# Performance work log

Hardware: AMD Instinct MI355X
Metric: run time of the kernel (lower is better)

Reference implementation:

```python
import jax, jax.numpy as jnp
import numpy as np

TEMPERATURE = 0.07
EPS = 1e-8  # torch F.cosine_similarity eps


def setup_inputs() -> dict:
    key = jax.random.key(0)
    k1, k2 = jax.random.split(key)
    N, D = 4096, 256
    z1 = jax.random.normal(k1, (N, D), dtype=jnp.float32)
    z2 = jax.random.normal(k2, (N, D), dtype=jnp.float32)
    return {"z1": z1, "z2": z2}


def reference(z1, z2):
    N = z1.shape[0]
    z = jnp.concatenate([z1, z2], axis=0)  # (2N, D)
    # cosine similarity = normalize(z) @ normalize(z).T (with eps clamp on norms)
    norms = jnp.maximum(jnp.linalg.norm(z, axis=-1, keepdims=True), EPS)
    zn = z / norms
    sim = (zn @ zn.T) / TEMPERATURE  # (2N, 2N)
    twoN = 2 * N
    eye = jnp.eye(twoN, dtype=bool)
    sim = jnp.where(eye, -1e9, sim)
    pos = jnp.concatenate([jnp.arange(N, twoN), jnp.arange(0, N)])
    # cross entropy with integer targets, mean reduction
    logZ = jax.nn.logsumexp(sim, axis=-1)  # (2N,)
    pos_logit = jnp.take_along_axis(sim, pos[:, None], axis=1)[:, 0]
    loss = jnp.mean(logZ - pos_logit)
    return loss
```

## Files before the change

kernel.cpp:

```cpp
#include <hip/hip_runtime.h>

#define N2   8192
#define DDIM 256
#define NBLK 32
#define NTRI 528

static constexpr float INV_T = 1.0f / 0.07f;

using bf16x8 = __attribute__((ext_vector_type(8))) __bf16;
using f32x4  = __attribute__((ext_vector_type(4))) float;
using u16x4  = __attribute__((ext_vector_type(4))) unsigned short;
typedef unsigned short u16;
typedef unsigned int   u32;

#define GL2LDS(gp, lp) __builtin_amdgcn_global_load_lds( \
    (const __attribute__((address_space(1))) void*)(gp), \
    (__attribute__((address_space(3))) void*)(lp), 16, 0, 0)

__device__ __forceinline__ u16 f2bf(float f) {
    u32 u = __float_as_uint(f);
    u32 r = (u + 0x7fffu + ((u >> 16) & 1u)) >> 16;
    return (u16)r;
}

__global__ void ntx_norm(const float* __restrict__ z1, const float* __restrict__ z2,
                         u16* __restrict__ zn)
{
    const int w    = threadIdx.x >> 6;
    const int lane = threadIdx.x & 63;
    const int row  = blockIdx.x * 4 + w;

    const float* src = (row < 4096) ? (z1 + (size_t)row * DDIM)
                                    : (z2 + (size_t)(row - 4096) * DDIM);
    float4 v = *(const float4*)(src + lane * 4);
    float ss = v.x * v.x + v.y * v.y + v.z * v.z + v.w * v.w;
    #pragma unroll
    for (int m = 1; m < 64; m <<= 1) ss += __shfl_xor(ss, m, 64);

    float inv = 1.0f / fmaxf(sqrtf(ss), 1e-8f);

    u16x4 o;
    o.x = f2bf(v.x * inv); o.y = f2bf(v.y * inv);
    o.z = f2bf(v.z * inv); o.w = f2bf(v.w * inv);
    *(u16x4*)(zn + (size_t)row * DDIM + lane * 4) = o;
}

__global__ __launch_bounds__(512, 2)
void ntx_gemm(const u16* __restrict__ zn, float* __restrict__ rowp,
              float* __restrict__ colp, float* __restrict__ pos)
{
    __shared__ u16 lsA[2][16384];
    __shared__ u16 lsB[2][16384];

    const int tid  = threadIdx.x;
    const int lane = tid & 63;
    const int w    = tid >> 6;
    const int wr   = w >> 2;
    const int wc   = w & 3;

    const int t = (int)blockIdx.x;
    int br = (int)((65.0f - sqrtf(4225.0f - 8.0f * (float)t)) * 0.5f);
    while ((br + 1) * (65 - (br + 1)) / 2 <= t) ++br;
    while (br * (65 - br) / 2 > t) --br;
    const int bc = br + (t - br * (65 - br) / 2);

    const int fr  = lane & 15;
    const int kl  = lane >> 4;
    const int swz = (fr & 7) << 4;

    const int srow = w * 8 + (lane >> 3);
    const int scsw = ((lane & 7) * 16) ^ ((lane >> 3) << 4);

    auto stage = [&](int buf, int kt) {
        const char* gA = (const char*)zn + (size_t)(br * 256 + srow) * 512 + kt * 128 + scsw;
        const char* gB = (const char*)zn + (size_t)(bc * 256 + srow) * 512 + kt * 128 + scsw;
        u16* lA = &lsA[buf][w * 512];
        u16* lB = &lsB[buf][w * 512];
        #pragma unroll
        for (int i = 0; i < 4; ++i) {
            GL2LDS(gA + (size_t)i * 32768, lA + i * 4096);
            GL2LDS(gB + (size_t)i * 32768, lB + i * 4096);
        }
    };

    f32x4 acc[8][4] = {};

    stage(0, 0);
    __syncthreads();

    #pragma unroll
    for (int kt = 0; kt < 4; ++kt) {
        const int buf = kt & 1;
        if (kt < 3) stage(buf ^ 1, kt + 1);
        #pragma unroll
        for (int ks = 0; ks < 2; ++ks) {
            const int kb = ks * 64 + kl * 16;
            bf16x8 af[8], bv[4];
            #pragma unroll
            for (int mf = 0; mf < 8; ++mf) {
                const int r = wr * 128 + mf * 16 + fr;
                af[mf] = *(const bf16x8*)((const char*)&lsA[buf][0] + r * 128 + (kb ^ swz));
            }
            #pragma unroll
            for (int nf = 0; nf < 4; ++nf) {
                const int c = wc * 64 + nf * 16 + fr;
                bv[nf] = *(const bf16x8*)((const char*)&lsB[buf][0] + c * 128 + (kb ^ swz));
            }
            #pragma unroll
            for (int mf = 0; mf < 8; ++mf)
                #pragma unroll
                for (int nf = 0; nf < 4; ++nf)
                    acc[mf][nf] = __builtin_amdgcn_mfma_f32_16x16x32_bf16(
                        af[mf], bv[nf], acc[mf][nf], 0, 0, 0);
        }
        __syncthreads();
    }

    const bool diag   = (br == bc);
    const bool posblk = (bc == br + 16);
    float colsum[4] = {0.f, 0.f, 0.f, 0.f};

    #pragma unroll
    for (int mf = 0; mf < 8; ++mf) {
        float rs[4] = {0.f, 0.f, 0.f, 0.f};
        const int rloc0 = wr * 128 + mf * 16 + kl * 4;
        #pragma unroll
        for (int nf = 0; nf < 4; ++nf) {
            const int cloc = wc * 64 + nf * 16 + fr;
            f32x4 a = acc[mf][nf];
            #pragma unroll
            for (int j = 0; j < 4; ++j) {
                const int rloc = rloc0 + j;
                float e = (diag && rloc == cloc) ? 0.f : __expf((a[j] - 1.0f) * INV_T);
                rs[j]      += e;
                colsum[nf] += e;
                if (posblk && rloc == cloc) {
                    const int grow = br * 256 + rloc;
                    pos[grow]        = a[j];
                    pos[grow + 4096] = a[j];
                }
            }
        }
        #pragma unroll
        for (int m = 1; m < 16; m <<= 1) {
            #pragma unroll
            for (int j = 0; j < 4; ++j) rs[j] += __shfl_xor(rs[j], m, 64);
        }
        if (fr == 0) {
            float* p = rowp + (size_t)(br * 256 + rloc0) * 128 + bc * 4 + wc;
            #pragma unroll
            for (int j = 0; j < 4; ++j) p[j * 128] = rs[j];
        }
    }

    if (!diag) {
        #pragma unroll
        for (int m = 16; m < 64; m <<= 1) {
            #pragma unroll
            for (int nf = 0; nf < 4; ++nf) colsum[nf] += __shfl_xor(colsum[nf], m, 64);
        }
        if (kl == 0) {
            #pragma unroll
            for (int nf = 0; nf < 4; ++nf) {
                const int col = bc * 256 + wc * 64 + nf * 16 + fr;
                colp[(size_t)col * 64 + br * 2 + wr] = colsum[nf];
            }
        }
    }
}

__global__ void ntx_loss(const float* __restrict__ rowp, const float* __restrict__ colp,
                         const float* __restrict__ pos, float* __restrict__ loss)
{
    const int w    = threadIdx.x >> 6;
    const int lane = threadIdx.x & 63;
    const int row  = blockIdx.x * 4 + w;
    const int R    = row >> 8;

    float s = 0.f;
    float v0 = rowp[(size_t)row * 128 + lane];
    float v1 = rowp[(size_t)row * 128 + 64 + lane];
    float v2 = colp[(size_t)row * 64 + lane];
    if (lane      >= 4 * R) s += v0;
    if (lane + 64 >= 4 * R) s += v1;
    if (lane      <  2 * R) s += v2;

    #pragma unroll
    for (int m = 1; m < 64; m <<= 1) s += __shfl_xor(s, m, 64);

    if (lane == 0)
        loss[row] = __logf(s) + INV_T - pos[row] * INV_T;
}

__global__ void ntx_reduce(const float* __restrict__ loss, float* __restrict__ out)
{
    __shared__ float sm[1024];
    const int t = threadIdx.x;
    float s = 0.f;
    for (int i = t; i < N2; i += 1024) s += loss[i];
    sm[t] = s;
    __syncthreads();
    for (int wdt = 512; wdt > 0; wdt >>= 1) {
        if (t < wdt) sm[t] += sm[t + wdt];
        __syncthreads();
    }
    if (t == 0) out[0] = sm[0] * (1.0f / (float)N2);
}

extern "C" void kernel_launch(void* const* d_in, const int* in_sizes, int n_in,
                              void* d_out, int out_size, void* d_ws, size_t ws_size,
                              hipStream_t stream)
{
    const float* z1 = (const float*)d_in[0];
    const float* z2 = (const float*)d_in[1];
    float* out = (float*)d_out;

    u16*   zn   = (u16*)d_ws;
    float* rowp = (float*)((char*)d_ws + (4u << 20));
    float* colp = (float*)((char*)d_ws + (8u << 20));
    float* loss = (float*)((char*)d_ws + (10u << 20));
    float* pos  = loss + N2;

    ntx_norm  <<<N2 / 4, 256, 0, stream>>>(z1, z2, zn);
    ntx_gemm  <<<NTRI, 512, 0, stream>>>(zn, rowp, colp, pos);
    ntx_loss  <<<N2 / 4, 256, 0, stream>>>(rowp, colp, pos, loss);
    ntx_reduce<<<1, 1024, 0, stream>>>(loss, out);
}
```

Before: 57.70 us.

## Prefetch two K-tiles ahead with explicit vmcnt waits and raw barriers

Both LDS buffers are filled at the start, and each buffer is refilled two K-steps ahead once its compute finishes. Partial s_waitcnt vmcnt counts replace the full __syncthreads drain, so one tile's global-to-LDS loads can stay in flight while the next tile is computed. The aim is to hide global load latency in the short four-step K loop. Correctness now depends on the hand-counted vmcnt values, and the barriers and sched_barriers may limit instruction interleaving.

Measured after the change: 56.95 us. About the same (-1.3%).

```diff
diff --git a/kernel.cpp b/kernel.cpp
--- a/kernel.cpp
+++ b/kernel.cpp
@@ -2,7 +2,6 @@
 
 #define N2   8192
 #define DDIM 256
-#define NBLK 32
 #define NTRI 528
 
 static constexpr float INV_T = 1.0f / 0.07f;
@@ -86,12 +85,18 @@
     f32x4 acc[8][4] = {};
 
     stage(0, 0);
-    __syncthreads();
+    stage(1, 1);
+    asm volatile("s_waitcnt vmcnt(8)" ::: "memory");
+    __builtin_amdgcn_sched_barrier(0);
+    __builtin_amdgcn_s_barrier();
+    __builtin_amdgcn_sched_barrier(0);
 
     #pragma unroll
     for (int kt = 0; kt < 4; ++kt) {
         const int buf = kt & 1;
-        if (kt < 3) stage(buf ^ 1, kt + 1);
+        const char* A = (const char*)&lsA[buf][0];
+        const char* B = (const char*)&lsB[buf][0];
+
         #pragma unroll
         for (int ks = 0; ks < 2; ++ks) {
             const int kb = ks * 64 + kl * 16;
@@ -99,12 +104,12 @@
             #pragma unroll
             for (int mf = 0; mf < 8; ++mf) {
                 const int r = wr * 128 + mf * 16 + fr;
-                af[mf] = *(const bf16x8*)((const char*)&lsA[buf][0] + r * 128 + (kb ^ swz));
+                af[mf] = *(const bf16x8*)(A + r * 128 + (kb ^ swz));
             }
             #pragma unroll
             for (int nf = 0; nf < 4; ++nf) {
                 const int c = wc * 64 + nf * 16 + fr;
-                bv[nf] = *(const bf16x8*)((const char*)&lsB[buf][0] + c * 128 + (kb ^ swz));
+                bv[nf] = *(const bf16x8*)(B + c * 128 + (kb ^ swz));
             }
             #pragma unroll
             for (int mf = 0; mf < 8; ++mf)
@@ -113,7 +118,23 @@
                     acc[mf][nf] = __builtin_amdgcn_mfma_f32_16x16x32_bf16(
                         af[mf], bv[nf], acc[mf][nf], 0, 0, 0);
         }
-        __syncthreads();
+
+        if (kt < 2) {
+            asm volatile("s_waitcnt lgkmcnt(0)" ::: "memory");
+            __builtin_amdgcn_sched_barrier(0);
+            __builtin_amdgcn_s_barrier();
+            __builtin_amdgcn_sched_barrier(0);
+            stage(buf, kt + 2);
+            asm volatile("s_waitcnt vmcnt(8)" ::: "memory");
+            __builtin_amdgcn_sched_barrier(0);
+            __builtin_amdgcn_s_barrier();
+            __builtin_amdgcn_sched_barrier(0);
+        } else if (kt == 2) {
+            asm volatile("s_waitcnt vmcnt(0)" ::: "memory");
+            __builtin_amdgcn_sched_barrier(0);
+            __builtin_amdgcn_s_barrier();
+            __builtin_amdgcn_sched_barrier(0);
+        }
     }
 
     const bool diag   = (br == bc);
```
